# Kernel tuning notes

Measured on AMD Instinct MI355X. Metric: run time of the kernel, lower is better.

The kernel has to match this reference:

```python
import jax, jax.numpy as jnp
import numpy as np

NUM_QUBITS = 24
NUM_QUBITS_GATE = 2
NUM_STEPS = 8
GATE_DIM = 2 ** NUM_QUBITS_GATE  # 4


def setup_inputs() -> dict:
    key = jax.random.key(0)
    k1, k2 = jax.random.split(key)
    # state: stacked (real, imag) parts, shape (2,) + (2,)*NUM_QUBITS
    state = jax.random.normal(k1, (2,) + (2,) * NUM_QUBITS, dtype=jnp.float32)
    state = state / jnp.sqrt(jnp.sum(state * state))  # normalize amplitudes
    # gates: per-step complex 4x4 matrices as stacked (real, imag)
    gates = jax.random.normal(k2, (NUM_STEPS, 2, GATE_DIM, GATE_DIM), dtype=jnp.float32)
    # targets: two distinct qubit indices per step (deterministic, in-range)
    targets = np.array([[s % NUM_QUBITS, (s + 7) % NUM_QUBITS] for s in range(NUM_STEPS)], dtype=np.int64)
    return {"state": state, "gates": gates, "targets": jnp.asarray(targets)}


def _apply_circuit(state, gates, targets_np, n, g):
    G = 2 ** g
    dims = list(range(n))
    for step in range(targets_np.shape[0]):
        target = [int(q) for q in targets_np[step]]
        target_axes = [n - 1 - q for q in target]
        target_axes = list(reversed(target_axes))
        permutation = [i for i in dims if i not in target_axes] + target_axes
        permutation = [0] + [i + 1 for i in permutation]  # keep complex axis first
        inv_permutation = [0] * (n + 1)
        for i, d in enumerate(permutation):
            inv_permutation[d] = i
        # bring target qubit axes to the end, flatten the rest
        st = jnp.transpose(state, permutation).reshape(2, -1, G)  # (2, B, G)
        gr, gi = gates[step, 0], gates[step, 1]  # (G, G) real/imag
        sr, si = st[0], st[1]                    # (B, G)
        # complex matmul: out = gate @ s  (s laid out as (B, G) -> s @ gate.T)
        out_r = sr @ gr.T - si @ gi.T
        out_i = sr @ gi.T + si @ gr.T
        out = jnp.stack([out_r, out_i])          # (2, B, G)
        state = jnp.transpose(out.reshape((2,) + (2,) * n), inv_permutation)
    return state


def reference(state, gates, targets):
    targets_np = np.asarray(targets)  # concrete indices drive the (static) permutations
    return _apply_circuit(state, gates, targets_np, NUM_QUBITS, NUM_QUBITS_GATE)
```

## Files before the change

kernel.cpp:

```cpp
#include <hip/hip_runtime.h>

#define NSTATE (1 << 24)

__device__ __forceinline__ int padi(int a) { return a + (a >> 4); }

template<int L0, int L1, int GROUPS>
__device__ __forceinline__ void gate_step(float2* amp, const float* g, int tid) {
    float gr[16], gi[16];
#pragma unroll
    for (int j = 0; j < 16; ++j) { gr[j] = g[j]; gi[j] = g[16 + j]; }
#pragma unroll
    for (int k = 0; k < GROUPS; ++k) {
        int grp = tid + (k << 8);
        int lo  = grp & ((1 << L0) - 1);
        int mid = (grp >> L0) & ((1 << (L1 - L0 - 1)) - 1);
        int hi  = grp >> (L1 - 1);
        int a0  = lo | (mid << (L0 + 1)) | (hi << (L1 + 1));
        float2 x[4];
#pragma unroll
        for (int h = 0; h < 4; ++h) {
            int a = a0 | ((h & 1) << L0) | ((h >> 1) << L1);
            x[h] = amp[padi(a)];
        }
        float2 y[4];
#pragma unroll
        for (int o = 0; o < 4; ++o) {
            float yr = 0.f, yi = 0.f;
#pragma unroll
            for (int h = 0; h < 4; ++h) {
                float a_ = gr[o * 4 + h], b_ = gi[o * 4 + h];
                yr = fmaf(a_, x[h].x, yr);
                yr = fmaf(-b_, x[h].y, yr);
                yi = fmaf(a_, x[h].y, yi);
                yi = fmaf(b_, x[h].x, yi);
            }
            y[o] = make_float2(yr, yi);
        }
#pragma unroll
        for (int h = 0; h < 4; ++h) {
            int a = a0 | ((h & 1) << L0) | ((h >> 1) << L1);
            amp[padi(a)] = y[h];
        }
    }
}

__global__ void __launch_bounds__(256) qsim_passA(const float* in, float* out,
                                                  const float* gates) {
    __shared__ float2 amp[2048 + (2048 >> 4)];
    const int tid  = threadIdx.x;
    const int base = blockIdx.x << 11;
    const float* inr = in;
    const float* ini = in + NSTATE;
#pragma unroll
    for (int k = 0; k < 2; ++k) {
        int t = (tid + (k << 8)) << 2;
        float4 r = *(const float4*)(inr + base + t);
        float4 m = *(const float4*)(ini + base + t);
        int p = padi(t);
        amp[p + 0] = make_float2(r.x, m.x);
        amp[p + 1] = make_float2(r.y, m.y);
        amp[p + 2] = make_float2(r.z, m.z);
        amp[p + 3] = make_float2(r.w, m.w);
    }
    __syncthreads();
    gate_step<0, 7, 2>(amp, gates + 0 * 32, tid); __syncthreads();
    gate_step<1, 8, 2>(amp, gates + 1 * 32, tid); __syncthreads();
    gate_step<2, 9, 2>(amp, gates + 2 * 32, tid); __syncthreads();
    gate_step<3, 10, 2>(amp, gates + 3 * 32, tid); __syncthreads();
#pragma unroll
    for (int k = 0; k < 2; ++k) {
        int t = (tid + (k << 8)) << 2;
        int p = padi(t);
        float2 c0 = amp[p + 0], c1 = amp[p + 1], c2 = amp[p + 2], c3 = amp[p + 3];
        *(float4*)(out + base + t)          = make_float4(c0.x, c1.x, c2.x, c3.x);
        *(float4*)(out + NSTATE + base + t) = make_float4(c0.y, c1.y, c2.y, c3.y);
    }
}

__global__ void __launch_bounds__(256) qsim_passB(const float* in, float* out,
                                                  const float* gates) {
    __shared__ float2 amp[4096 + (4096 >> 4)];
    const int tid = threadIdx.x;
    const int bid = blockIdx.x;
    const int base = ((bid & 7) << 8) | ((bid >> 3) << 15);
    const float* inr = in;
    const float* ini = in + NSTATE;
#pragma unroll
    for (int k = 0; k < 4; ++k) {
        int c = (k << 2) + (tid >> 6);
        int j = (tid & 63) << 2;
        int t = (c << 8) + j;
        int ga = base + (c << 11) + j;
        float4 r = *(const float4*)(inr + ga);
        float4 m = *(const float4*)(ini + ga);
        int p = padi(t);
        amp[p + 0] = make_float2(r.x, m.x);
        amp[p + 1] = make_float2(r.y, m.y);
        amp[p + 2] = make_float2(r.z, m.z);
        amp[p + 3] = make_float2(r.w, m.w);
    }
    __syncthreads();
    gate_step<4, 8, 4>(amp, gates + 4 * 32, tid); __syncthreads();
    gate_step<5, 9, 4>(amp, gates + 5 * 32, tid); __syncthreads();
    gate_step<6, 10, 4>(amp, gates + 6 * 32, tid); __syncthreads();
    gate_step<7, 11, 4>(amp, gates + 7 * 32, tid); __syncthreads();
#pragma unroll
    for (int k = 0; k < 4; ++k) {
        int c = (k << 2) + (tid >> 6);
        int j = (tid & 63) << 2;
        int t = (c << 8) + j;
        int ga = base + (c << 11) + j;
        int p = padi(t);
        float2 c0 = amp[p + 0], c1 = amp[p + 1], c2 = amp[p + 2], c3 = amp[p + 3];
        *(float4*)(out + ga)          = make_float4(c0.x, c1.x, c2.x, c3.x);
        *(float4*)(out + NSTATE + ga) = make_float4(c0.y, c1.y, c2.y, c3.y);
    }
}

extern "C" void kernel_launch(void* const* d_in, const int* in_sizes, int n_in,
                              void* d_out, int out_size, void* d_ws, size_t ws_size,
                              hipStream_t stream) {
    const float* state = (const float*)d_in[0];
    const float* gates = (const float*)d_in[1];
    float* out = (float*)d_out;
    hipLaunchKernelGGL(qsim_passA, dim3(8192), dim3(256), 0, stream, state, out, gates);
    hipLaunchKernelGGL(qsim_passB, dim3(4096), dim3(256), 0, stream, out, out, gates);
}
```

Baseline: 279.7 us.

## Fuse both passes into one kernel with register-resident amplitudes and lane shuffles

Replaces the two shared-memory kernels with a single kernel where each 1024-thread block owns a 2^15-amplitude tile. Each thread holds 32 amplitudes in registers, and gates act across lanes via xor shuffles or within a thread. A swizzled shared-memory transpose between the gate groups remaps qubits. This halves global memory traffic by avoiding the intermediate write and read of the state, at the cost of scalar (non-vectorized) global loads, high register pressure and only 512 blocks.

New measurement: 405.5 us. 45.0% more time.

```diff
diff --git a/kernel.cpp b/kernel.cpp
--- a/kernel.cpp
+++ b/kernel.cpp
@@ -2,118 +2,101 @@
 
 #define NSTATE (1 << 24)
 
-__device__ __forceinline__ int padi(int a) { return a + (a >> 4); }
 
-template<int L0, int L1, int GROUPS>
-__device__ __forceinline__ void gate_step(float2* amp, const float* g, int tid) {
-    float gr[16], gi[16];
+__device__ __forceinline__ float2 shfl2(float2 v, int mask) {
+    return make_float2(__shfl_xor(v.x, mask, 64), __shfl_xor(v.y, mask, 64));
+}
+
+__device__ __forceinline__ void cfma(float2& y, float2 c, float2 x) {
+    y.x = fmaf(c.x, x.x, y.x);
+    y.x = fmaf(-c.y, x.y, y.x);
+    y.y = fmaf(c.x, x.y, y.y);
+    y.y = fmaf(c.y, x.x, y.y);
+}
+
+__device__ __forceinline__ int swz(int l) { return l ^ (((l >> 4) & 3) << 2); }
+
+template<int MASK, int D>
+__device__ __forceinline__ void applyGate(float2* amp, const float* __restrict__ g,
+                                          int lane) {
+    const bool b = (lane & MASK) != 0;
+    float2 c00 = b ? make_float2(g[5],  g[21]) : make_float2(g[0],  g[16]);
+    float2 c01 = b ? make_float2(g[4],  g[20]) : make_float2(g[1],  g[17]);
+    float2 c02 = b ? make_float2(g[7],  g[23]) : make_float2(g[2],  g[18]);
+    float2 c03 = b ? make_float2(g[6],  g[22]) : make_float2(g[3],  g[19]);
+    float2 c10 = b ? make_float2(g[13], g[29]) : make_float2(g[8],  g[24]);
+    float2 c11 = b ? make_float2(g[12], g[28]) : make_float2(g[9],  g[25]);
+    float2 c12 = b ? make_float2(g[15], g[31]) : make_float2(g[10], g[26]);
+    float2 c13 = b ? make_float2(g[14], g[30]) : make_float2(g[11], g[27]);
 #pragma unroll
-    for (int j = 0; j < 16; ++j) { gr[j] = g[j]; gi[j] = g[16 + j]; }
-#pragma unroll
-    for (int k = 0; k < GROUPS; ++k) {
-        int grp = tid + (k << 8);
-        int lo  = grp & ((1 << L0) - 1);
-        int mid = (grp >> L0) & ((1 << (L1 - L0 - 1)) - 1);
-        int hi  = grp >> (L1 - 1);
-        int a0  = lo | (mid << (L0 + 1)) | (hi << (L1 + 1));
-        float2 x[4];
-#pragma unroll
-        for (int h = 0; h < 4; ++h) {
-            int a = a0 | ((h & 1) << L0) | ((h >> 1) << L1);
-            x[h] = amp[padi(a)];
-        }
-        float2 y[4];
-#pragma unroll
-        for (int o = 0; o < 4; ++o) {
-            float yr = 0.f, yi = 0.f;
-#pragma unroll
-            for (int h = 0; h < 4; ++h) {
-                float a_ = gr[o * 4 + h], b_ = gi[o * 4 + h];
-                yr = fmaf(a_, x[h].x, yr);
-                yr = fmaf(-b_, x[h].y, yr);
-                yi = fmaf(a_, x[h].y, yi);
-                yi = fmaf(b_, x[h].x, yi);
-            }
-            y[o] = make_float2(yr, yi);
-        }
-#pragma unroll
-        for (int h = 0; h < 4; ++h) {
-            int a = a0 | ((h & 1) << L0) | ((h >> 1) << L1);
-            amp[padi(a)] = y[h];
-        }
+    for (int u = 0; u < 16; ++u) {
+        const int h = (u & (D - 1)) | ((u & ~(D - 1)) << 1);
+        float2 A0 = amp[h], A1 = amp[h | D];
+        float2 B0 = shfl2(A0, MASK), B1 = shfl2(A1, MASK);
+        float2 y0 = make_float2(0.f, 0.f), y1 = make_float2(0.f, 0.f);
+        cfma(y0, c00, A0); cfma(y0, c01, B0); cfma(y0, c02, A1); cfma(y0, c03, B1);
+        cfma(y1, c10, A0); cfma(y1, c11, B0); cfma(y1, c12, A1); cfma(y1, c13, B1);
+        amp[h] = y0; amp[h | D] = y1;
     }
 }
 
-__global__ void __launch_bounds__(256) qsim_passA(const float* in, float* out,
-                                                  const float* gates) {
-    __shared__ float2 amp[2048 + (2048 >> 4)];
+__global__ void __launch_bounds__(1024) qsim_fused(const float* __restrict__ in,
+                                                   float* __restrict__ out,
+                                                   const float* __restrict__ gates) {
+    __shared__ float2 xch[8192];
+    float2 amp[32];
     const int tid  = threadIdx.x;
-    const int base = blockIdx.x << 11;
-    const float* inr = in;
-    const float* ini = in + NSTATE;
+    const int lane = tid & 63;
+    const int warp = tid >> 6;
+    const int blockBase = (int)blockIdx.x << 15;
+    const int m1 = blockBase | lane | ((warp & 1) << 6) | (((warp >> 1) & 1) << 11)
+                 | (((warp >> 2) & 1) << 12) | ((warp >> 3) << 13);
+    const int lwb = lane | ((warp & 1) << 6) | ((warp >> 1) << 10);
+    const int lrb = (lane & 3) | ((warp & 3) << 2) | (((lane >> 2) & 0xF) << 4)
+                  | ((warp >> 2) << 8);
+    const float* re = in;
+    const float* im = in + NSTATE;
 #pragma unroll
-    for (int k = 0; k < 2; ++k) {
-        int t = (tid + (k << 8)) << 2;
-        float4 r = *(const float4*)(inr + base + t);
-        float4 m = *(const float4*)(ini + base + t);
-        int p = padi(t);
-        amp[p + 0] = make_float2(r.x, m.x);
-        amp[p + 1] = make_float2(r.y, m.y);
-        amp[p + 2] = make_float2(r.z, m.z);
-        amp[p + 3] = make_float2(r.w, m.w);
+    for (int h = 0; h < 32; ++h) {
+        const int off = ((h & 1) << 7) | (((h >> 1) & 1) << 8) | (((h >> 2) & 1) << 9)
+                      | (((h >> 3) & 1) << 10) | (((h >> 4) & 1) << 14);
+        amp[h].x = re[m1 + off];
+        amp[h].y = im[m1 + off];
     }
-    __syncthreads();
-    gate_step<0, 7, 2>(amp, gates + 0 * 32, tid); __syncthreads();
-    gate_step<1, 8, 2>(amp, gates + 1 * 32, tid); __syncthreads();
-    gate_step<2, 9, 2>(amp, gates + 2 * 32, tid); __syncthreads();
-    gate_step<3, 10, 2>(amp, gates + 3 * 32, tid); __syncthreads();
+    applyGate<1, 1>(amp, gates + 0,  lane);
+    applyGate<2, 2>(amp, gates + 32, lane);
+    applyGate<4, 4>(amp, gates + 64, lane);
+    applyGate<8, 8>(amp, gates + 96, lane);
 #pragma unroll
-    for (int k = 0; k < 2; ++k) {
-        int t = (tid + (k << 8)) << 2;
-        int p = padi(t);
-        float2 c0 = amp[p + 0], c1 = amp[p + 1], c2 = amp[p + 2], c3 = amp[p + 3];
-        *(float4*)(out + base + t)          = make_float4(c0.x, c1.x, c2.x, c3.x);
-        *(float4*)(out + NSTATE + base + t) = make_float4(c0.y, c1.y, c2.y, c3.y);
+    for (int c = 0; c < 4; ++c) {
+#pragma unroll
+        for (int i = 0; i < 8; ++i) xch[swz(lwb | (i << 7))] = amp[8 * c + i];
+        __syncthreads();
+#pragma unroll
+        for (int i = 0; i < 8; ++i) amp[8 * c + i] = xch[swz(lrb | (i << 10))];
+        __syncthreads();
     }
-}
-
-__global__ void __launch_bounds__(256) qsim_passB(const float* in, float* out,
-                                                  const float* gates) {
-    __shared__ float2 amp[4096 + (4096 >> 4)];
-    const int tid = threadIdx.x;
-    const int bid = blockIdx.x;
-    const int base = ((bid & 7) << 8) | ((bid >> 3) << 15);
-    const float* inr = in;
-    const float* ini = in + NSTATE;
+    applyGate<4,  1>(amp, gates + 128, lane);
+    applyGate<8,  2>(amp, gates + 160, lane);
+    applyGate<16, 4>(amp, gates + 192, lane);
+    applyGate<32, 16>(amp, gates + 224, lane);
 #pragma unroll
-    for (int k = 0; k < 4; ++k) {
-        int c = (k << 2) + (tid >> 6);
-        int j = (tid & 63) << 2;
-        int t = (c << 8) + j;
-        int ga = base + (c << 11) + j;
-        float4 r = *(const float4*)(inr + ga);
-        float4 m = *(const float4*)(ini + ga);
-        int p = padi(t);
-        amp[p + 0] = make_float2(r.x, m.x);
-        amp[p + 1] = make_float2(r.y, m.y);
-        amp[p + 2] = make_float2(r.z, m.z);
-        amp[p + 3] = make_float2(r.w, m.w);
+    for (int c = 0; c < 4; ++c) {
+#pragma unroll
+        for (int i = 0; i < 8; ++i) xch[swz(lrb | (i << 10))] = amp[8 * c + i];
+        __syncthreads();
+#pragma unroll
+        for (int i = 0; i < 8; ++i) amp[8 * c + i] = xch[swz(lwb | (i << 7))];
+        __syncthreads();
     }
-    __syncthreads();
-    gate_step<4, 8, 4>(amp, gates + 4 * 32, tid); __syncthreads();
-    gate_step<5, 9, 4>(amp, gates + 5 * 32, tid); __syncthreads();
-    gate_step<6, 10, 4>(amp, gates + 6 * 32, tid); __syncthreads();
-    gate_step<7, 11, 4>(amp, gates + 7 * 32, tid); __syncthreads();
+    float* ore = out;
+    float* oim = out + NSTATE;
 #pragma unroll
-    for (int k = 0; k < 4; ++k) {
-        int c = (k << 2) + (tid >> 6);
-        int j = (tid & 63) << 2;
-        int t = (c << 8) + j;
-        int ga = base + (c << 11) + j;
-        int p = padi(t);
-        float2 c0 = amp[p + 0], c1 = amp[p + 1], c2 = amp[p + 2], c3 = amp[p + 3];
-        *(float4*)(out + ga)          = make_float4(c0.x, c1.x, c2.x, c3.x);
-        *(float4*)(out + NSTATE + ga) = make_float4(c0.y, c1.y, c2.y, c3.y);
+    for (int h = 0; h < 32; ++h) {
+        const int off = ((h & 1) << 7) | (((h >> 1) & 1) << 8) | (((h >> 2) & 1) << 9)
+                      | (((h >> 3) & 1) << 10) | (((h >> 4) & 1) << 14);
+        ore[m1 + off] = amp[h].x;
+        oim[m1 + off] = amp[h].y;
     }
 }
 
@@ -123,6 +106,5 @@
     const float* state = (const float*)d_in[0];
     const float* gates = (const float*)d_in[1];
     float* out = (float*)d_out;
-    hipLaunchKernelGGL(qsim_passA, dim3(8192), dim3(256), 0, stream, state, out, gates);
-    hipLaunchKernelGGL(qsim_passB, dim3(4096), dim3(256), 0, stream, out, out, gates);
+    hipLaunchKernelGGL(qsim_fused, dim3(512), dim3(1024), 0, stream, state, out, gates);
 }
```
